# Kernel tuning notes

Measured on AMD Instinct MI355X. Metric: run time of the kernel, lower is better.

Reference implementation:

```python
import jax, jax.numpy as jnp
import numpy as np
from jax.scipy.special import logsumexp

EPS = 1.0
MAX_ITER = 50


def setup_inputs() -> dict:
    key = jax.random.key(0)
    k1, k2 = jax.random.split(key)
    x = jax.random.uniform(k1, (2048, 32), dtype=jnp.float32)
    y = jax.random.uniform(k2, (2048, 32), dtype=jnp.float32)
    return {"x": x, "y": y}


def _sinkhorn_loss(x, y):
    # cost[i, j] = sum_k |x[i,k] - y[j,k]|^2   -> [N, M]
    cost = jnp.sum(jnp.square(x[:, None, :] - y[None, :, :]), axis=-1)
    neg_cost_over_eps = -cost / EPS

    def step(log_alpha, _):
        # symmetric normalization via row/col logsumexp
        log_alpha = log_alpha - 0.5 * (
            logsumexp(log_alpha, axis=0, keepdims=True)
            + logsumexp(log_alpha, axis=1, keepdims=True)
        )
        # faithful to the original: raw log of row-sum (not stabilized)
        log_alpha = log_alpha - jnp.log(
            jnp.sum(jnp.exp(neg_cost_over_eps - log_alpha), axis=1, keepdims=True)
        )
        return log_alpha, None

    log_alpha0 = jnp.zeros_like(cost)
    log_alpha, _ = jax.lax.scan(step, log_alpha0, None, length=MAX_ITER)
    P = jnp.exp(log_alpha)
    return jnp.sum(P * cost)


def reference(x, y):
    return _sinkhorn_loss(x, y)
```

## Files before the change

### kernel.cpp

```cpp
#include <hip/hip_runtime.h>

#define NPTS 2048
#define DIM  32
#define RPB  4
#define T1   256
#define T2   256
#define LOG_M 7.6246189861593985

__global__ __launch_bounds__(T1)
void sink_rowstats(const float* __restrict__ x, const float* __restrict__ y,
                   float* __restrict__ R, float* __restrict__ Crow) {
    __shared__ float redE[RPB][T1 / 64];
    __shared__ float redC[RPB][T1 / 64];

    const int tid = threadIdx.x;
    const int rowBase = blockIdx.x * RPB;

    float xr[RPB][DIM];
    float xn[RPB];
#pragma unroll
    for (int r = 0; r < RPB; ++r) {
        const float4* xp = (const float4*)(x + (rowBase + r) * DIM);
        float s = 0.f;
#pragma unroll
        for (int q = 0; q < DIM / 4; ++q) {
            float4 v = xp[q];
            xr[r][4*q+0] = v.x; xr[r][4*q+1] = v.y;
            xr[r][4*q+2] = v.z; xr[r][4*q+3] = v.w;
            s = fmaf(v.x, v.x, fmaf(v.y, v.y, fmaf(v.z, v.z, fmaf(v.w, v.w, s))));
        }
        xn[r] = s;
    }

    float accE[RPB], accC[RPB];
#pragma unroll
    for (int r = 0; r < RPB; ++r) { accE[r] = 0.f; accC[r] = 0.f; }

    for (int j = tid; j < NPTS; j += T1) {
        const float4* yp = (const float4*)(y + j * DIM);
        float yv[DIM];
        float yn = 0.f;
#pragma unroll
        for (int q = 0; q < DIM / 4; ++q) {
            float4 v = yp[q];
            yv[4*q+0] = v.x; yv[4*q+1] = v.y;
            yv[4*q+2] = v.z; yv[4*q+3] = v.w;
            yn = fmaf(v.x, v.x, fmaf(v.y, v.y, fmaf(v.z, v.z, fmaf(v.w, v.w, yn))));
        }
#pragma unroll
        for (int r = 0; r < RPB; ++r) {
            float dot = 0.f;
#pragma unroll
            for (int k = 0; k < DIM; ++k)
                dot = fmaf(xr[r][k], yv[k], dot);
            float c = fmaf(-2.f, dot, xn[r] + yn);
            accE[r] += __expf(-c);
            accC[r] += c;
        }
    }

#pragma unroll
    for (int r = 0; r < RPB; ++r) {
#pragma unroll
        for (int off = 32; off >= 1; off >>= 1) {
            accE[r] += __shfl_xor(accE[r], off, 64);
            accC[r] += __shfl_xor(accC[r], off, 64);
        }
    }
    const int wave = tid >> 6;
    if ((tid & 63) == 0) {
#pragma unroll
        for (int r = 0; r < RPB; ++r) {
            redE[r][wave] = accE[r];
            redC[r][wave] = accC[r];
        }
    }
    __syncthreads();
    if (tid < RPB) {
        float e = 0.f, c = 0.f;
#pragma unroll
        for (int wv = 0; wv < T1 / 64; ++wv) { e += redE[tid][wv]; c += redC[tid][wv]; }
        R[rowBase + tid]    = e;
        Crow[rowBase + tid] = c;
    }
}

__global__ __launch_bounds__(T2)
void sink_finish(const float* __restrict__ R, const float* __restrict__ Crow,
                 float* __restrict__ out) {
    __shared__ float  smf[T2 / 64];
    __shared__ double smd[T2 / 64];
    const int tid = threadIdx.x;
    const int lane = tid & 63, wave = tid >> 6;
    const int NW = T2 / 64;

    float w[NPTS / T2];
    float cr[NPTS / T2];
#pragma unroll
    for (int r = 0; r < NPTS / T2; ++r) {
        int i = tid + r * T2;
        w[r]  = (float)LOG_M + logf(R[i]);
        cr[r] = Crow[i];
    }

    float m = -49.f * w[0];
#pragma unroll
    for (int r = 1; r < NPTS / T2; ++r) m = fmaxf(m, -49.f * w[r]);
#pragma unroll
    for (int off = 32; off >= 1; off >>= 1) m = fmaxf(m, __shfl_xor(m, off, 64));
    if (lane == 0) smf[wave] = m;
    __syncthreads();
    m = smf[0];
#pragma unroll
    for (int wv = 1; wv < NW; ++wv) m = fmaxf(m, smf[wv]);
    __syncthreads();

    double s = 0.0;
#pragma unroll
    for (int r = 0; r < NPTS / T2; ++r)
        s += (double)__expf(fmaf(-49.f, w[r], -m));
#pragma unroll
    for (int off = 32; off >= 1; off >>= 1) s += __shfl_xor(s, off, 64);
    if (lane == 0) smd[wave] = s;
    __syncthreads();
    s = 0.0;
#pragma unroll
    for (int wv = 0; wv < NW; ++wv) s += smd[wv];
    const float c50 = m + logf((float)s);
    __syncthreads();

    double loss = 0.0;
#pragma unroll
    for (int r = 0; r < NPTS / T2; ++r)
        loss += (double)__expf(fmaf(-50.f, w[r], -c50)) * (double)cr[r];
#pragma unroll
    for (int off = 32; off >= 1; off >>= 1) loss += __shfl_xor(loss, off, 64);
    if (lane == 0) smd[wave] = loss;
    __syncthreads();
    if (tid == 0) {
        double t = 0.0;
#pragma unroll
        for (int wv = 0; wv < NW; ++wv) t += smd[wv];
        out[0] = (float)t;
    }
}

extern "C" void kernel_launch(void* const* d_in, const int* in_sizes, int n_in,
                              void* d_out, int out_size, void* d_ws, size_t ws_size,
                              hipStream_t stream) {
    const float* x = (const float*)d_in[0];
    const float* y = (const float*)d_in[1];
    float* out = (float*)d_out;
    float* ws  = (float*)d_ws;
    float* R    = ws;
    float* Crow = ws + NPTS;

    sink_rowstats<<<NPTS / RPB, T1, 0, stream>>>(x, y, R, Crow);
    sink_finish<<<1, T2, 0, stream>>>(R, Crow, out);
}
```

Baseline: 25.40 us.

## Fuse row-stats and finish kernels into one cooperative launch with grid sync

Merges the two kernels into a single cooperative kernel. Each of the 512 blocks writes its row statistics, then a grid-wide sync lets block 0 do the final log-sum-exp reduction. This removes a second kernel launch and the gap between launches. In exchange it pays for a grid barrier and requires all 512 blocks to be co-resident (launch bounds set to 2 blocks per CU), and cooperative launch carries its own overhead.

```diff
diff --git a/kernel.cpp b/kernel.cpp
--- a/kernel.cpp
+++ b/kernel.cpp
@@ -1,111 +1,119 @@
 #include <hip/hip_runtime.h>
+#include <hip/hip_cooperative_groups.h>
+
+namespace cg = cooperative_groups;
 
 #define NPTS 2048
 #define DIM  32
 #define RPB  4
-#define T1   256
-#define T2   256
+#define T    256
+#define NBLK (NPTS / RPB)
+#define EPT  (NPTS / T)
 #define LOG_M 7.6246189861593985
 
-__global__ __launch_bounds__(T1)
-void sink_rowstats(const float* __restrict__ x, const float* __restrict__ y,
-                   float* __restrict__ R, float* __restrict__ Crow) {
-    __shared__ float redE[RPB][T1 / 64];
-    __shared__ float redC[RPB][T1 / 64];
+__global__ __launch_bounds__(T, 2)
+void sink_fused(const float* __restrict__ x, const float* __restrict__ y,
+                float* __restrict__ ws, float* __restrict__ out) {
+    float* R    = ws;
+    float* Crow = ws + NPTS;
 
-    const int tid = threadIdx.x;
-    const int rowBase = blockIdx.x * RPB;
+    __shared__ float  redE[RPB][T / 64];
+    __shared__ float  redC[RPB][T / 64];
+    __shared__ float  smf[T / 64];
+    __shared__ double smd[T / 64];
 
-    float xr[RPB][DIM];
-    float xn[RPB];
-#pragma unroll
-    for (int r = 0; r < RPB; ++r) {
-        const float4* xp = (const float4*)(x + (rowBase + r) * DIM);
-        float s = 0.f;
-#pragma unroll
-        for (int q = 0; q < DIM / 4; ++q) {
-            float4 v = xp[q];
-            xr[r][4*q+0] = v.x; xr[r][4*q+1] = v.y;
-            xr[r][4*q+2] = v.z; xr[r][4*q+3] = v.w;
-            s = fmaf(v.x, v.x, fmaf(v.y, v.y, fmaf(v.z, v.z, fmaf(v.w, v.w, s))));
-        }
-        xn[r] = s;
-    }
+    const int tid  = threadIdx.x;
+    const int bid  = blockIdx.x;
+    const int lane = tid & 63, wave = tid >> 6;
+    const int NW   = T / 64;
 
-    float accE[RPB], accC[RPB];
-#pragma unroll
-    for (int r = 0; r < RPB; ++r) { accE[r] = 0.f; accC[r] = 0.f; }
+    {
+        const int rowBase = bid * RPB;
 
-    for (int j = tid; j < NPTS; j += T1) {
-        const float4* yp = (const float4*)(y + j * DIM);
-        float yv[DIM];
-        float yn = 0.f;
-#pragma unroll
-        for (int q = 0; q < DIM / 4; ++q) {
-            float4 v = yp[q];
-            yv[4*q+0] = v.x; yv[4*q+1] = v.y;
-            yv[4*q+2] = v.z; yv[4*q+3] = v.w;
-            yn = fmaf(v.x, v.x, fmaf(v.y, v.y, fmaf(v.z, v.z, fmaf(v.w, v.w, yn))));
-        }
+        float xr[RPB][DIM];
+        float xn[RPB];
 #pragma unroll
         for (int r = 0; r < RPB; ++r) {
-            float dot = 0.f;
+            const float4* xp = (const float4*)(x + (rowBase + r) * DIM);
+            float s = 0.f;
 #pragma unroll
-            for (int k = 0; k < DIM; ++k)
-                dot = fmaf(xr[r][k], yv[k], dot);
-            float c = fmaf(-2.f, dot, xn[r] + yn);
-            accE[r] += __expf(-c);
-            accC[r] += c;
+            for (int q = 0; q < DIM / 4; ++q) {
+                float4 v = xp[q];
+                xr[r][4*q+0] = v.x; xr[r][4*q+1] = v.y;
+                xr[r][4*q+2] = v.z; xr[r][4*q+3] = v.w;
+                s = fmaf(v.x, v.x, fmaf(v.y, v.y, fmaf(v.z, v.z, fmaf(v.w, v.w, s))));
+            }
+            xn[r] = s;
+        }
+
+        float accE[RPB], accC[RPB];
+#pragma unroll
+        for (int r = 0; r < RPB; ++r) { accE[r] = 0.f; accC[r] = 0.f; }
+
+        for (int j = tid; j < NPTS; j += T) {
+            const float4* yp = (const float4*)(y + j * DIM);
+            float yv[DIM];
+            float yn = 0.f;
+#pragma unroll
+            for (int q = 0; q < DIM / 4; ++q) {
+                float4 v = yp[q];
+                yv[4*q+0] = v.x; yv[4*q+1] = v.y;
+                yv[4*q+2] = v.z; yv[4*q+3] = v.w;
+                yn = fmaf(v.x, v.x, fmaf(v.y, v.y, fmaf(v.z, v.z, fmaf(v.w, v.w, yn))));
+            }
+#pragma unroll
+            for (int r = 0; r < RPB; ++r) {
+                float dot = 0.f;
+#pragma unroll
+                for (int k = 0; k < DIM; ++k)
+                    dot = fmaf(xr[r][k], yv[k], dot);
+                float c = fmaf(-2.f, dot, xn[r] + yn);
+                accE[r] += __expf(-c);
+                accC[r] += c;
+            }
+        }
+
+#pragma unroll
+        for (int r = 0; r < RPB; ++r) {
+#pragma unroll
+            for (int off = 32; off >= 1; off >>= 1) {
+                accE[r] += __shfl_xor(accE[r], off, 64);
+                accC[r] += __shfl_xor(accC[r], off, 64);
+            }
+        }
+        if (lane == 0) {
+#pragma unroll
+            for (int r = 0; r < RPB; ++r) {
+                redE[r][wave] = accE[r];
+                redC[r][wave] = accC[r];
+            }
+        }
+        __syncthreads();
+        if (tid < RPB) {
+            float e = 0.f, c = 0.f;
+#pragma unroll
+            for (int wv = 0; wv < NW; ++wv) { e += redE[tid][wv]; c += redC[tid][wv]; }
+            R[rowBase + tid]    = e;
+            Crow[rowBase + tid] = c;
         }
     }
 
+    __threadfence();
+    cg::this_grid().sync();
+
+    if (bid != 0) return;
+
+    float w[EPT], cr[EPT];
 #pragma unroll
-    for (int r = 0; r < RPB; ++r) {
-#pragma unroll
-        for (int off = 32; off >= 1; off >>= 1) {
-            accE[r] += __shfl_xor(accE[r], off, 64);
-            accC[r] += __shfl_xor(accC[r], off, 64);
-        }
-    }
-    const int wave = tid >> 6;
-    if ((tid & 63) == 0) {
-#pragma unroll
-        for (int r = 0; r < RPB; ++r) {
-            redE[r][wave] = accE[r];
-            redC[r][wave] = accC[r];
-        }
-    }
-    __syncthreads();
-    if (tid < RPB) {
-        float e = 0.f, c = 0.f;
-#pragma unroll
-        for (int wv = 0; wv < T1 / 64; ++wv) { e += redE[tid][wv]; c += redC[tid][wv]; }
-        R[rowBase + tid]    = e;
-        Crow[rowBase + tid] = c;
-    }
-}
-
-__global__ __launch_bounds__(T2)
-void sink_finish(const float* __restrict__ R, const float* __restrict__ Crow,
-                 float* __restrict__ out) {
-    __shared__ float  smf[T2 / 64];
-    __shared__ double smd[T2 / 64];
-    const int tid = threadIdx.x;
-    const int lane = tid & 63, wave = tid >> 6;
-    const int NW = T2 / 64;
-
-    float w[NPTS / T2];
-    float cr[NPTS / T2];
-#pragma unroll
-    for (int r = 0; r < NPTS / T2; ++r) {
-        int i = tid + r * T2;
+    for (int r = 0; r < EPT; ++r) {
+        int i = tid + r * T;
         w[r]  = (float)LOG_M + logf(R[i]);
         cr[r] = Crow[i];
     }
 
     float m = -49.f * w[0];
 #pragma unroll
-    for (int r = 1; r < NPTS / T2; ++r) m = fmaxf(m, -49.f * w[r]);
+    for (int r = 1; r < EPT; ++r) m = fmaxf(m, -49.f * w[r]);
 #pragma unroll
     for (int off = 32; off >= 1; off >>= 1) m = fmaxf(m, __shfl_xor(m, off, 64));
     if (lane == 0) smf[wave] = m;
@@ -117,7 +125,7 @@
 
     double s = 0.0;
 #pragma unroll
-    for (int r = 0; r < NPTS / T2; ++r)
+    for (int r = 0; r < EPT; ++r)
         s += (double)__expf(fmaf(-49.f, w[r], -m));
 #pragma unroll
     for (int off = 32; off >= 1; off >>= 1) s += __shfl_xor(s, off, 64);
@@ -131,7 +139,7 @@
 
     double loss = 0.0;
 #pragma unroll
-    for (int r = 0; r < NPTS / T2; ++r)
+    for (int r = 0; r < EPT; ++r)
         loss += (double)__expf(fmaf(-50.f, w[r], -c50)) * (double)cr[r];
 #pragma unroll
     for (int off = 32; off >= 1; off >>= 1) loss += __shfl_xor(loss, off, 64);
@@ -152,9 +160,8 @@
     const float* y = (const float*)d_in[1];
     float* out = (float*)d_out;
     float* ws  = (float*)d_ws;
-    float* R    = ws;
-    float* Crow = ws + NPTS;
 
-    sink_rowstats<<<NPTS / RPB, T1, 0, stream>>>(x, y, R, Crow);
-    sink_finish<<<1, T2, 0, stream>>>(R, Crow, out);
+    void* args[] = {(void*)&x, (void*)&y, (void*)&ws, (void*)&out};
+    hipLaunchCooperativeKernel((const void*)sink_fused, dim3(NBLK), dim3(T),
+                               args, 0, stream);
 }
```

After: 90.29 us. 256% more time.
